# Kernel optimization log

Hardware: AMD Instinct MI355X
Metric: run time of the kernel (lower is better)

Reference implementation:

```python
import jax, jax.numpy as jnp
import numpy as np

B, S, D, H = 4, 2048, 1024, 16
DH = D // H
SCALE = float(np.sqrt(DH))


def setup_inputs() -> dict:
    key = jax.random.key(0)
    ks = jax.random.split(key, 5)
    std = 1.0 / np.sqrt(D)
    return {
        "x": jax.random.normal(ks[0], (B, S, D), dtype=jnp.float32),
        "Wq": jax.random.normal(ks[1], (D, D), dtype=jnp.float32) * std,
        "bq": jnp.zeros((D,), dtype=jnp.float32),
        "Wk": jax.random.normal(ks[2], (D, D), dtype=jnp.float32) * std,
        "bk": jnp.zeros((D,), dtype=jnp.float32),
        "Wv": jax.random.normal(ks[3], (D, D), dtype=jnp.float32) * std,
        "bv": jnp.zeros((D,), dtype=jnp.float32),
        "Wo": jax.random.normal(ks[4], (D, D), dtype=jnp.float32) * std,
        "bo": jnp.zeros((D,), dtype=jnp.float32),
        "padding_mask": jnp.ones((B, S), dtype=jnp.int32),
    }


def reference(x, Wq, bq, Wk, bk, Wv, bv, Wo, bo, padding_mask):
    b, s, d = x.shape
    # QKV projections, split heads -> [b, h, s, dh]
    q = (x @ Wq + bq).reshape(b, s, H, DH).transpose(0, 2, 1, 3)
    k = (x @ Wk + bk).reshape(b, s, H, DH).transpose(0, 2, 1, 3)
    v = (x @ Wv + bv).reshape(b, s, H, DH).transpose(0, 2, 1, 3)
    # scaled scores [b, h, s, s]
    scores = jnp.einsum('bhqd,bhkd->bhqk', q, k) / SCALE
    neg_inf = jnp.float32(-jnp.inf)
    causal = jnp.tril(jnp.ones((s, s), dtype=bool))  # [s, s]
    scores = jnp.where(causal[None, None, :, :], scores, neg_inf)
    pad = (padding_mask != 0)[:, None, None, :]  # [b,1,1,s] on key axis
    scores = jnp.where(pad, scores, neg_inf)
    weights = jax.nn.softmax(scores, axis=-1)
    weights = jnp.nan_to_num(weights, nan=0.0)  # fully-masked rows -> 0
    # dropout is identity in eval / p=0
    attended = jnp.einsum('bhqk,bhkd->bhqd', weights, v)
    attended = attended.transpose(0, 2, 1, 3).reshape(b, s, d)
    return attended @ Wo + bo
```

## Files before the change

kernel.cpp:

```cpp
#include <hip/hip_runtime.h>
#include <hip/hip_bf16.h>

#define B_   4
#define S_   2048
#define D_   1024
#define H_   16
#define DH_  64
#define M_   (B_ * S_)

typedef __attribute__((ext_vector_type(8))) short  bfrag8;
typedef __attribute__((ext_vector_type(4))) float  facc4;
typedef unsigned short u16;
typedef unsigned long long u64;

__device__ __forceinline__ u16 f2bf(float f) {
    union { __hip_bfloat16 h; u16 u; } c;
    c.h = __float2bfloat16(f);
    return c.u;
}

__device__ __forceinline__ u16 bfr(float f) {
    unsigned b = __float_as_uint(f);
    return (u16)((b + 0x7FFFu + ((b >> 16) & 1u)) >> 16);
}

__device__ __forceinline__ void gl_lds16(const u16* g, u16* l) {
    __builtin_amdgcn_global_load_lds((const __attribute__((address_space(1))) void*)g,
                                     (__attribute__((address_space(3))) void*)l,
                                     16, 0, 0);
}

__global__ __launch_bounds__(256) void prep(const float* __restrict__ x, u16* __restrict__ X16,
                                            const float* __restrict__ w0, const float* __restrict__ w1,
                                            const float* __restrict__ w2, const float* __restrict__ w3,
                                            u16* __restrict__ o0, u16* __restrict__ o1,
                                            u16* __restrict__ o2, u16* __restrict__ o3) {
    __shared__ u16 t[32][33];
    int bid = blockIdx.x;
    if (bid < 4096) {
        int i = (bid * 256 + threadIdx.x) * 8;
        float4 v0 = *(const float4*)(x + i);
        float4 v1 = *(const float4*)(x + i + 4);
        ushort4 r0, r1;
        r0.x = f2bf(v0.x); r0.y = f2bf(v0.y); r0.z = f2bf(v0.z); r0.w = f2bf(v0.w);
        r1.x = f2bf(v1.x); r1.y = f2bf(v1.y); r1.z = f2bf(v1.z); r1.w = f2bf(v1.w);
        *(ushort4*)(X16 + i) = r0;
        *(ushort4*)(X16 + i + 4) = r1;
    } else {
        int lid = bid - 4096;
        int z = lid >> 10, r = lid & 1023;
        const float* w; u16* o;
        switch (z) {
            case 0: w = w0; o = o0; break;
            case 1: w = w1; o = o1; break;
            case 2: w = w2; o = o2; break;
            default: w = w3; o = o3; break;
        }
        int kb = (r >> 5) * 32, nb = (r & 31) * 32;
        int c = threadIdx.x & 31, r0 = threadIdx.x >> 5;
#pragma unroll
        for (int i = 0; i < 4; i++) {
            int rr = r0 + 8 * i;
            t[rr][c] = f2bf(w[(kb + rr) * D_ + nb + c]);
        }
        __syncthreads();
#pragma unroll
        for (int i = 0; i < 4; i++) {
            int rr = r0 + 8 * i;
            o[(nb + rr) * D_ + kb + c] = t[c][rr];
        }
    }
}

#define ABUF_ (256 * 64)
#define TBUF_ ((256 + 128) * 64)
#define NKT_  16

__device__ __forceinline__ void gemm_body256(const u16* __restrict__ A,
                                             const u16* __restrict__ BT,
                                             const float* __restrict__ bias,
                                             void* __restrict__ Cout, int mode, float scale,
                                             u16* S, int nb, int mb) {
    int tid = threadIdx.x;
    int w = tid >> 6, lane = tid & 63, quad = lane >> 4, l16 = lane & 15;
    int wm = (w >> 1) * 64, wn = (w & 1) * 64;
    int x7 = l16 & 7;

    const u16* Aga[4]; const u16* Bga[2];
#pragma unroll
    for (int i = 0; i < 4; ++i) {
        int idx = i * 512 + tid, row = idx >> 3;
        int lu = (idx & 7) ^ (row & 7);
        Aga[i] = A + (size_t)(mb + row) * D_ + lu * 8;
    }
#pragma unroll
    for (int i = 0; i < 2; ++i) {
        int idx = i * 512 + tid, row = idx >> 3;
        int lu = (idx & 7) ^ (row & 7);
        Bga[i] = BT + (size_t)(nb + row) * D_ + lu * 8;
    }

    facc4 acc[4][4] = {};

    u16* Bu0 = S;
    u16* Bu1 = S + TBUF_;
    u16* Bu2 = S + 2 * TBUF_;

    auto stage = [&](u16* Nb, int ko) {
#pragma unroll
        for (int i = 0; i < 4; ++i) gl_lds16(Aga[i] + ko, Nb + (i * 512 + tid) * 8);
#pragma unroll
        for (int i = 0; i < 2; ++i) gl_lds16(Bga[i] + ko, Nb + ABUF_ + (i * 512 + tid) * 8);
    };
    auto compute = [&](const u16* Cb) {
#pragma unroll
        for (int k2 = 0; k2 < 2; ++k2) {
            int pu = ((k2 * 4 + quad) ^ x7) * 8;
            bfrag8 af[4], bf[4];
#pragma unroll
            for (int mt = 0; mt < 4; ++mt)
                af[mt] = *(const bfrag8*)(Cb + (wm + mt * 16 + l16) * 64 + pu);
#pragma unroll
            for (int nt = 0; nt < 4; ++nt)
                bf[nt] = *(const bfrag8*)(Cb + ABUF_ + (wn + nt * 16 + l16) * 64 + pu);
            __builtin_amdgcn_s_setprio(1);
#pragma unroll
            for (int mt = 0; mt < 4; ++mt)
#pragma unroll
                for (int nt = 0; nt < 4; ++nt)
                    acc[mt][nt] = __builtin_amdgcn_mfma_f32_16x16x32_bf16(af[mt], bf[nt], acc[mt][nt], 0, 0, 0);
            __builtin_amdgcn_s_setprio(0);
        }
    };

    stage(Bu0, 0);
    stage(Bu1, 64);

    u16 *bc = Bu0, *bn = Bu1, *bs = Bu2;
    for (int kt = 0; kt < NKT_; ++kt) {
        if (kt < NKT_ - 1) asm volatile("s_waitcnt vmcnt(6)" ::: "memory");
        else               asm volatile("s_waitcnt vmcnt(0)" ::: "memory");
        __builtin_amdgcn_sched_barrier(0);
        __builtin_amdgcn_s_barrier();
        __builtin_amdgcn_sched_barrier(0);
        if (kt + 2 < NKT_) stage(bs, (kt + 2) * 64);
        compute(bc);
        u16* tmp = bc; bc = bn; bn = bs; bs = tmp;
    }

#pragma unroll
    for (int mt = 0; mt < 4; ++mt) {
        int m_base = mb + wm + mt * 16 + quad * 4;
#pragma unroll
        for (int nt = 0; nt < 4; ++nt) {
            int n = nb + wn + nt * 16 + l16;
            float bv = bias[n];
            int h = n >> 6, dd = n & 63;
#pragma unroll
            for (int r = 0; r < 4; ++r) {
                int m = m_base + r;
                float v = (acc[mt][nt][r] + bv) * scale;
                int bi = m >> 11, s = m & (S_ - 1);
                if (mode == 0) {
                    ((u16*)Cout)[(((bi * H_ + h) * S_) + s) * DH_ + dd] = bfr(v);
                } else if (mode == 1) {
                    ((u16*)Cout)[(((bi * H_ + h) * DH_) + dd) * S_ + s] = bfr(v);
                } else {
                    ((float*)Cout)[(size_t)m * D_ + n] = v;
                }
            }
        }
    }
}

#define CE_Q 0.18033688011112042f

__global__ __launch_bounds__(512, 1) void gemm_qkv(const u16* __restrict__ A,
                                                const u16* __restrict__ WTq, const float* __restrict__ bq, u16* __restrict__ Qb,
                                                const u16* __restrict__ WTk, const float* __restrict__ bk, u16* __restrict__ Kb,
                                                const u16* __restrict__ WTv, const float* __restrict__ bv, u16* __restrict__ VTb) {
    __shared__ __attribute__((aligned(16))) u16 Sh[3 * TBUF_];
    int lid = blockIdx.x;
    int xcd = lid & 7, s = lid >> 3;
    int z = s >> 5, inner = s & 31;
    int mb = (xcd * 4 + (inner >> 3)) * 256;
    int nb = (inner & 7) * 128;
    switch (z) {
        case 0: gemm_body256(A, WTq, bq, Qb, 0, CE_Q, Sh, nb, mb); break;
        case 1: gemm_body256(A, WTk, bk, Kb, 0, 1.0f, Sh, nb, mb); break;
        default: gemm_body256(A, WTv, bv, VTb, 1, 1.0f, Sh, nb, mb); break;
    }
}

__global__ __launch_bounds__(512, 1) void gemm_o(const u16* __restrict__ A,
                                              const u16* __restrict__ WTo, const float* __restrict__ bo,
                                              float* __restrict__ out) {
    __shared__ __attribute__((aligned(16))) u16 Sh[3 * TBUF_];
    int lid = blockIdx.x;
    int xcd = lid & 7, s = lid >> 3;
    int mb = (xcd * 4 + (s >> 3)) * 256;
    int nb = (s & 7) * 128;
    gemm_body256(A, WTo, bo, out, 2, 1.0f, Sh, nb, mb);
}

__device__ __forceinline__ void soft_pv(const float* p, float& lp, facc4* oaccq,
                                        const bfrag8* vf, int a0, int a1, bool qlo) {
    float rs = 0.f;
    unsigned pk[4];
#pragma unroll
    for (int j = 0; j < 4; ++j) {
        float e0 = exp2f(p[2 * j]);
        float e1 = exp2f(p[2 * j + 1]);
        rs += e0; rs += e1;
        pk[j] = __builtin_amdgcn_perm(__float_as_uint(e1), __float_as_uint(e0), 0x07060302u);
    }
    lp += rs;
    union { unsigned d[4]; bfrag8 v; } pb;
    {
        unsigned lo, hi;
        lo = __builtin_amdgcn_ds_bpermute(a0, (int)pk[0]);
        hi = __builtin_amdgcn_ds_bpermute(a0, (int)pk[2]);
        pb.d[0] = qlo ? lo : hi;
        lo = __builtin_amdgcn_ds_bpermute(a0, (int)pk[1]);
        hi = __builtin_amdgcn_ds_bpermute(a0, (int)pk[3]);
        pb.d[1] = qlo ? lo : hi;
        lo = __builtin_amdgcn_ds_bpermute(a1, (int)pk[0]);
        hi = __builtin_amdgcn_ds_bpermute(a1, (int)pk[2]);
        pb.d[2] = qlo ? lo : hi;
        lo = __builtin_amdgcn_ds_bpermute(a1, (int)pk[1]);
        hi = __builtin_amdgcn_ds_bpermute(a1, (int)pk[3]);
        pb.d[3] = qlo ? lo : hi;
    }
    __builtin_amdgcn_s_setprio(1);
#pragma unroll
    for (int dt = 0; dt < 4; ++dt)
        oaccq[dt] = __builtin_amdgcn_mfma_f32_16x16x32_bf16(vf[dt], pb.v, oaccq[dt], 0, 0, 0);
    __builtin_amdgcn_s_setprio(0);
}

__global__ __launch_bounds__(256, 4) void attn(const u16* __restrict__ Q,
                                               const u16* __restrict__ K,
                                               const u16* __restrict__ VT,
                                               const int* __restrict__ pm,
                                               u16* __restrict__ Aout) {
    __shared__ __attribute__((aligned(16))) u16 Ks[2][32 * 64];
    __shared__ __attribute__((aligned(16))) u16 Vs[2][64 * 32];
    __shared__ unsigned pms[64];

    int tid = threadIdx.x, w = tid >> 6, lane = tid & 63;
    int quad = lane >> 4, l16 = lane & 15;

    int lid = blockIdx.x;
    int bh  = (lid & 7) * 8 + ((lid >> 3) & 7);
    int g   = lid >> 6;
    int gq = g >> 2, gr = g & 3;
    int ci = (gq == 0) ? 15 - gr : (gq == 1) ? gr : (gq == 2) ? 11 - gr : 4 + gr;
    int b = bh >> 4, h = bh & 15;

    int qbase = ci * 128;
    int qw = qbase + w * 32;
    int tmax = (qbase >> 5) + 3;

    const u16* Qp = Q + (size_t)(b * H_ + h) * S_ * DH_;
    const u16* Kp = K + (size_t)(b * H_ + h) * S_ * DH_;
    const u16* Vp = VT + (size_t)(b * H_ + h) * DH_ * S_;
    u16* Ao = Aout + (size_t)b * S_ * D_ + h * DH_;

#pragma unroll
    for (int i = 0; i < 8; ++i) {
        int j2 = w * 16 + i * 2;
        u64 m = __ballot(pm[b * S_ + j2 * 32 + lane] != 0);
        if (lane == 0) { pms[j2] = (unsigned)m; pms[j2 + 1] = (unsigned)(m >> 32); }
    }

    int krow = tid >> 3, ku = tid & 7;
    const u16* Kg = Kp + krow * DH_ + ((ku ^ (krow & 7)) * 8);
    int vrow = tid >> 2, vu = tid & 3;
    const u16* Vg = Vp + vrow * S_ + ((vu ^ (vrow & 3)) * 8);
    u16* Kl[2] = { &Ks[0][tid * 8], &Ks[1][tid * 8] };
    u16* Vl[2] = { &Vs[0][tid * 8], &Vs[1][tid * 8] };

    int k7 = l16 & 7, v3 = l16 & 3;

    int a0 = ((((2 * quad) & 3) * 16 + l16) << 2);
    int a1 = ((((2 * quad + 1) & 3) * 16 + l16) << 2);
    bool qlo = quad < 2;

    bfrag8 qf[2][2];
#pragma unroll
    for (int qt = 0; qt < 2; ++qt)
#pragma unroll
        for (int cc = 0; cc < 2; ++cc)
            qf[qt][cc] = *(const bfrag8*)(Qp + (qw + qt * 16 + l16) * DH_ + cc * 32 + quad * 8);

    facc4 oacc[2][4] = {};
    float lp[2] = {0.f, 0.f};

    gl_lds16(Kg, Kl[0]);
    gl_lds16(Vg, Vl[0]);
    __syncthreads();
    unsigned vmn = pms[0];

    for (int t = 0; t <= tmax; ++t) {
        int cur = t & 1, nxt = cur ^ 1;
        unsigned vm = vmn;
        if (t < tmax) {
            int k1 = (t + 1) * 32;
            gl_lds16(Kg + k1 * DH_, Kl[nxt]);
            gl_lds16(Vg + k1, Vl[nxt]);
            vmn = pms[t + 1];
        }
        int k0 = t * 32;
        const u16* Kc = Ks[cur];
        const u16* Vc = Vs[cur];

        bfrag8 kf00 = *(const bfrag8*)(Kc + (l16 * 8        + ((quad)     ^ k7)) * 8);
        bfrag8 kf01 = *(const bfrag8*)(Kc + (l16 * 8        + ((quad + 4) ^ k7)) * 8);
        bfrag8 kf10 = *(const bfrag8*)(Kc + ((l16 + 16) * 8 + ((quad)     ^ k7)) * 8);
        bfrag8 kf11 = *(const bfrag8*)(Kc + ((l16 + 16) * 8 + ((quad + 4) ^ k7)) * 8);
        bfrag8 vf[4];
#pragma unroll
        for (int dt = 0; dt < 4; ++dt)
            vf[dt] = *(const bfrag8*)(Vc + ((dt * 16 + l16) * 4 + (quad ^ v3)) * 8);

        facc4 st[2][2] = {};
        __builtin_amdgcn_s_setprio(1);
#pragma unroll
        for (int qt = 0; qt < 2; ++qt) {
            st[qt][0] = __builtin_amdgcn_mfma_f32_16x16x32_bf16(kf00, qf[qt][0], st[qt][0], 0, 0, 0);
            st[qt][0] = __builtin_amdgcn_mfma_f32_16x16x32_bf16(kf01, qf[qt][1], st[qt][0], 0, 0, 0);
            st[qt][1] = __builtin_amdgcn_mfma_f32_16x16x32_bf16(kf10, qf[qt][0], st[qt][1], 0, 0, 0);
            st[qt][1] = __builtin_amdgcn_mfma_f32_16x16x32_bf16(kf11, qf[qt][1], st[qt][1], 0, 0, 0);
        }
        __builtin_amdgcn_s_setprio(0);

        if (vm == 0xffffffffu && k0 + 31 < qw) {
#pragma unroll
            for (int qt = 0; qt < 2; ++qt) {
                float p[8];
#pragma unroll
                for (int kt = 0; kt < 2; ++kt)
#pragma unroll
                    for (int r = 0; r < 4; ++r) p[kt * 4 + r] = st[qt][kt][r];
                soft_pv(p, lp[qt], oacc[qt], vf, a0, a1, qlo);
            }
        } else {
#pragma unroll
            for (int qt = 0; qt < 2; ++qt) {
                int q0 = qw + qt * 16;
                float p[8];
#pragma unroll
                for (int kt = 0; kt < 2; ++kt)
#pragma unroll
                    for (int r = 0; r < 4; ++r) {
                        int kl = kt * 16 + quad * 4 + r;
                        bool ok = ((vm >> kl) & 1u) && (k0 + kl <= q0 + l16);
                        p[kt * 4 + r] = ok ? st[qt][kt][r] : -1e30f;
                    }
                soft_pv(p, lp[qt], oacc[qt], vf, a0, a1, qlo);
            }
        }
        __syncthreads();
    }

#pragma unroll
    for (int qt = 0; qt < 2; ++qt) {
        float l = lp[qt];
        l += __shfl_xor(l, 16);
        l += __shfl_xor(l, 32);
        float linv = (l > 0.f) ? 1.f / l : 0.f;
        size_t qoff = (size_t)(qw + qt * 16 + l16) * D_;
#pragma unroll
        for (int dt = 0; dt < 4; ++dt) {
            union { u16 hh[4]; u64 q; } pk4;
#pragma unroll
            for (int r = 0; r < 4; ++r) pk4.hh[r] = bfr(oacc[qt][dt][r] * linv);
            *(u64*)(Ao + qoff + dt * 16 + quad * 4) = pk4.q;
        }
    }
}

extern "C" void kernel_launch(void* const* d_in, const int* in_sizes, int n_in,
                              void* d_out, int out_size, void* d_ws, size_t ws_size,
                              hipStream_t stream) {
    const float* x  = (const float*)d_in[0];
    const float* Wq = (const float*)d_in[1];
    const float* bq = (const float*)d_in[2];
    const float* Wk = (const float*)d_in[3];
    const float* bk = (const float*)d_in[4];
    const float* Wv = (const float*)d_in[5];
    const float* bv = (const float*)d_in[6];
    const float* Wo = (const float*)d_in[7];
    const float* bo = (const float*)d_in[8];
    const int*   pm = (const int*)d_in[9];
    float* out = (float*)d_out;

    char* ws = (char*)d_ws;
    const size_t SZ_XD = (size_t)M_ * D_ * 2;
    const size_t SZ_W  = (size_t)D_ * D_ * 2;
    u16* X16 = (u16*)ws;
    u16* WTq = (u16*)(ws + SZ_XD);
    u16* WTk = (u16*)(ws + SZ_XD + SZ_W);
    u16* WTv = (u16*)(ws + SZ_XD + 2 * SZ_W);
    u16* WTo = (u16*)(ws + SZ_XD + 3 * SZ_W);
    u16* Qb  = (u16*)(ws + SZ_XD + 4 * SZ_W);
    u16* Kb  = (u16*)(ws + 2 * SZ_XD + 4 * SZ_W);
    u16* VTb = (u16*)(ws + 3 * SZ_XD + 4 * SZ_W);
    u16* Att = X16;

    prep<<<dim3(8192), 256, 0, stream>>>(x, X16, Wq, Wk, Wv, Wo, WTq, WTk, WTv, WTo);

    gemm_qkv<<<dim3(768), 512, 0, stream>>>(X16, WTq, bq, Qb, WTk, bk, Kb, WTv, bv, VTb);

    attn<<<dim3(1024), 256, 0, stream>>>(Qb, Kb, VTb, pm, Att);

    gemm_o<<<dim3(256), 512, 0, stream>>>(Att, WTo, bo, out);
}
```

Measured before the change: 251.1 us.

## Triple-buffer K/V tiles in attention with partial vmcnt waits and causal tile skip

```diff
diff --git a/kernel.cpp b/kernel.cpp
--- a/kernel.cpp
+++ b/kernel.cpp
@@ -243,8 +243,8 @@
                                                const u16* __restrict__ VT,
                                                const int* __restrict__ pm,
                                                u16* __restrict__ Aout) {
-    __shared__ __attribute__((aligned(16))) u16 Ks[2][32 * 64];
-    __shared__ __attribute__((aligned(16))) u16 Vs[2][64 * 32];
+    __shared__ __attribute__((aligned(16))) u16 Ks[3][32 * 64];
+    __shared__ __attribute__((aligned(16))) u16 Vs[3][64 * 32];
     __shared__ unsigned pms[64];
 
     int tid = threadIdx.x, w = tid >> 6, lane = tid & 63;
@@ -277,8 +277,6 @@
     const u16* Kg = Kp + krow * DH_ + ((ku ^ (krow & 7)) * 8);
     int vrow = tid >> 2, vu = tid & 3;
     const u16* Vg = Vp + vrow * S_ + ((vu ^ (vrow & 3)) * 8);
-    u16* Kl[2] = { &Ks[0][tid * 8], &Ks[1][tid * 8] };
-    u16* Vl[2] = { &Vs[0][tid * 8], &Vs[1][tid * 8] };
 
     int k7 = l16 & 7, v3 = l16 & 3;
 
@@ -296,71 +294,90 @@
     facc4 oacc[2][4] = {};
     float lp[2] = {0.f, 0.f};
 
-    gl_lds16(Kg, Kl[0]);
-    gl_lds16(Vg, Vl[0]);
     __syncthreads();
+
+    u16 *kC = &Ks[0][0], *kN = &Ks[1][0], *kS = &Ks[2][0];
+    u16 *vC = &Vs[0][0], *vN = &Vs[1][0], *vS = &Vs[2][0];
+    gl_lds16(Kg, kC + tid * 8);
+    gl_lds16(Vg, vC + tid * 8);
+    gl_lds16(Kg + 32 * DH_, kN + tid * 8);
+    gl_lds16(Vg + 32, vN + tid * 8);
     unsigned vmn = pms[0];
+    asm volatile("s_waitcnt vmcnt(2) lgkmcnt(0)" ::: "memory");
+    __builtin_amdgcn_sched_barrier(0);
+    __builtin_amdgcn_s_barrier();
+    __builtin_amdgcn_sched_barrier(0);
 
     for (int t = 0; t <= tmax; ++t) {
-        int cur = t & 1, nxt = cur ^ 1;
         unsigned vm = vmn;
+        if (t < tmax) vmn = pms[t + 1];
+        if (t + 2 <= tmax) {
+            int kk = (t + 2) * 32;
+            gl_lds16(Kg + kk * DH_, kS + tid * 8);
+            gl_lds16(Vg + kk, vS + tid * 8);
+        }
+        int k0 = t * 32;
+
+        if (k0 <= qw + 31) {
+            const u16* Kc = kC;
+            const u16* Vc = vC;
+            bfrag8 kf00 = *(const bfrag8*)(Kc + (l16 * 8        + ((quad)     ^ k7)) * 8);
+            bfrag8 kf01 = *(const bfrag8*)(Kc + (l16 * 8        + ((quad + 4) ^ k7)) * 8);
+            bfrag8 kf10 = *(const bfrag8*)(Kc + ((l16 + 16) * 8 + ((quad)     ^ k7)) * 8);
+            bfrag8 kf11 = *(const bfrag8*)(Kc + ((l16 + 16) * 8 + ((quad + 4) ^ k7)) * 8);
+            bfrag8 vf[4];
+#pragma unroll
+            for (int dt = 0; dt < 4; ++dt)
+                vf[dt] = *(const bfrag8*)(Vc + ((dt * 16 + l16) * 4 + (quad ^ v3)) * 8);
+
+            facc4 st[2][2] = {};
+            __builtin_amdgcn_s_setprio(1);
+#pragma unroll
+            for (int qt = 0; qt < 2; ++qt) {
+                st[qt][0] = __builtin_amdgcn_mfma_f32_16x16x32_bf16(kf00, qf[qt][0], st[qt][0], 0, 0, 0);
+                st[qt][0] = __builtin_amdgcn_mfma_f32_16x16x32_bf16(kf01, qf[qt][1], st[qt][0], 0, 0, 0);
+                st[qt][1] = __builtin_amdgcn_mfma_f32_16x16x32_bf16(kf10, qf[qt][0], st[qt][1], 0, 0, 0);
+                st[qt][1] = __builtin_amdgcn_mfma_f32_16x16x32_bf16(kf11, qf[qt][1], st[qt][1], 0, 0, 0);
+            }
+            __builtin_amdgcn_s_setprio(0);
+
+            if (vm == 0xffffffffu && k0 + 31 < qw) {
+#pragma unroll
+                for (int qt = 0; qt < 2; ++qt) {
+                    float p[8];
+#pragma unroll
+                    for (int kt = 0; kt < 2; ++kt)
+#pragma unroll
+                        for (int r = 0; r < 4; ++r) p[kt * 4 + r] = st[qt][kt][r];
+                    soft_pv(p, lp[qt], oacc[qt], vf, a0, a1, qlo);
+                }
+            } else {
+#pragma unroll
+                for (int qt = 0; qt < 2; ++qt) {
+                    int q0 = qw + qt * 16;
+                    float p[8];
+#pragma unroll
+                    for (int kt = 0; kt < 2; ++kt)
+#pragma unroll
+                        for (int r = 0; r < 4; ++r) {
+                            int kl = kt * 16 + quad * 4 + r;
+                            bool ok = ((vm >> kl) & 1u) && (k0 + kl <= q0 + l16);
+                            p[kt * 4 + r] = ok ? st[qt][kt][r] : -1e30f;
+                        }
+                    soft_pv(p, lp[qt], oacc[qt], vf, a0, a1, qlo);
+                }
+            }
+        }
+
         if (t < tmax) {
-            int k1 = (t + 1) * 32;
-            gl_lds16(Kg + k1 * DH_, Kl[nxt]);
-            gl_lds16(Vg + k1, Vl[nxt]);
-            vmn = pms[t + 1];
-        }
-        int k0 = t * 32;
-        const u16* Kc = Ks[cur];
-        const u16* Vc = Vs[cur];
-
-        bfrag8 kf00 = *(const bfrag8*)(Kc + (l16 * 8        + ((quad)     ^ k7)) * 8);
-        bfrag8 kf01 = *(const bfrag8*)(Kc + (l16 * 8        + ((quad + 4) ^ k7)) * 8);
-        bfrag8 kf10 = *(const bfrag8*)(Kc + ((l16 + 16) * 8 + ((quad)     ^ k7)) * 8);
-        bfrag8 kf11 = *(const bfrag8*)(Kc + ((l16 + 16) * 8 + ((quad + 4) ^ k7)) * 8);
-        bfrag8 vf[4];
-#pragma unroll
-        for (int dt = 0; dt < 4; ++dt)
-            vf[dt] = *(const bfrag8*)(Vc + ((dt * 16 + l16) * 4 + (quad ^ v3)) * 8);
-
-        facc4 st[2][2] = {};
-        __builtin_amdgcn_s_setprio(1);
-#pragma unroll
-        for (int qt = 0; qt < 2; ++qt) {
-            st[qt][0] = __builtin_amdgcn_mfma_f32_16x16x32_bf16(kf00, qf[qt][0], st[qt][0], 0, 0, 0);
-            st[qt][0] = __builtin_amdgcn_mfma_f32_16x16x32_bf16(kf01, qf[qt][1], st[qt][0], 0, 0, 0);
-            st[qt][1] = __builtin_amdgcn_mfma_f32_16x16x32_bf16(kf10, qf[qt][0], st[qt][1], 0, 0, 0);
-            st[qt][1] = __builtin_amdgcn_mfma_f32_16x16x32_bf16(kf11, qf[qt][1], st[qt][1], 0, 0, 0);
-        }
-        __builtin_amdgcn_s_setprio(0);
-
-        if (vm == 0xffffffffu && k0 + 31 < qw) {
-#pragma unroll
-            for (int qt = 0; qt < 2; ++qt) {
-                float p[8];
-#pragma unroll
-                for (int kt = 0; kt < 2; ++kt)
-#pragma unroll
-                    for (int r = 0; r < 4; ++r) p[kt * 4 + r] = st[qt][kt][r];
-                soft_pv(p, lp[qt], oacc[qt], vf, a0, a1, qlo);
-            }
-        } else {
-#pragma unroll
-            for (int qt = 0; qt < 2; ++qt) {
-                int q0 = qw + qt * 16;
-                float p[8];
-#pragma unroll
-                for (int kt = 0; kt < 2; ++kt)
-#pragma unroll
-                    for (int r = 0; r < 4; ++r) {
-                        int kl = kt * 16 + quad * 4 + r;
-                        bool ok = ((vm >> kl) & 1u) && (k0 + kl <= q0 + l16);
-                        p[kt * 4 + r] = ok ? st[qt][kt][r] : -1e30f;
-                    }
-                soft_pv(p, lp[qt], oacc[qt], vf, a0, a1, qlo);
-            }
-        }
-        __syncthreads();
+            if (t + 2 <= tmax) asm volatile("s_waitcnt vmcnt(2) lgkmcnt(0)" ::: "memory");
+            else               asm volatile("s_waitcnt vmcnt(0) lgkmcnt(0)" ::: "memory");
+            __builtin_amdgcn_sched_barrier(0);
+            __builtin_amdgcn_s_barrier();
+            __builtin_amdgcn_sched_barrier(0);
+        }
+        u16* tk = kC; kC = kN; kN = kS; kS = tk;
+        u16* tv = vC; vC = vN; vN = vS; vS = tv;
     }
 
 #pragma unroll
```

Measured after the change: 259.5 us. 3.4% more time.
